# Kernel optimization log

Hardware: AMD Instinct MI355X
Metric: run time of the kernel (lower is better)

Reference implementation:

```python
import jax, jax.numpy as jnp
import numpy as np

N = 50000      # nodes
E = 600000     # edges
F_IN = 128     # input features
H = 128        # hidden
C = 40         # classes


def _glorot(key, shape):
    lim = float(np.sqrt(6.0 / (shape[0] + shape[1])))
    return jax.random.uniform(key, shape, jnp.float32, -lim, lim)


def setup_inputs() -> dict:
    key = jax.random.key(0)
    ks = jax.random.split(key, 16)
    inp = {
        "x": jax.random.normal(ks[0], (N, F_IN), jnp.float32),
        "edge_index": jax.random.randint(ks[1], (2, E), 0, N, jnp.int64),
    }
    # SAGEConv params: Wl (neighbor branch, with bias), Wr (root branch), stored [in, out]
    dims = [(F_IN, H), (H, H), (H, H)]
    for i, (din, dout) in enumerate(dims, start=1):
        inp[f"Wl{i}"] = _glorot(ks[2 * i], (din, dout))
        inp[f"bl{i}"] = jnp.zeros((dout,), jnp.float32)
        inp[f"Wr{i}"] = _glorot(ks[2 * i + 1], (din, dout))
    inp["W_lin1"] = _glorot(ks[10], (H, H))
    inp["b_lin1"] = jnp.zeros((H,), jnp.float32)
    inp["W_lin2"] = _glorot(ks[11], (H, C))
    inp["b_lin2"] = jnp.zeros((C,), jnp.float32)
    return inp


def _sage_conv(x, src, dst, Wl, bl, Wr):
    # mean-aggregate neighbor features at destination nodes
    msgs = x[src]  # [E, d] gather
    agg = jax.ops.segment_sum(msgs, dst, num_segments=N)
    deg = jax.ops.segment_sum(jnp.ones((E,), x.dtype), dst, num_segments=N)
    agg = agg / jnp.clip(deg, 1.0)[:, None]
    return agg @ Wl + bl + x @ Wr


def reference(x, edge_index, Wl1, bl1, Wr1, Wl2, bl2, Wr2, Wl3, bl3, Wr3,
              W_lin1, b_lin1, W_lin2, b_lin2):
    src, dst = edge_index[0], edge_index[1]
    h = jax.nn.relu(_sage_conv(x, src, dst, Wl1, bl1, Wr1))
    h = jax.nn.relu(_sage_conv(h, src, dst, Wl2, bl2, Wr2))
    h = jax.nn.relu(_sage_conv(h, src, dst, Wl3, bl3, Wr3))
    h = jax.nn.relu(h @ W_lin1 + b_lin1)
    # dropout: inference mode (training=False) -> identity
    logits = h @ W_lin2 + b_lin2
    return jax.nn.log_softmax(logits, axis=-1)
```

## Files before the change

### kernel.cpp

```cpp
#include <hip/hip_runtime.h>
#include <hip/hip_bf16.h>
#include <math.h>

#define NNODES 50000
#define NEDGES 600000
#define FDIM   128
#define NCLS   40
#define SLOTS  64
#define FILL_BLOCKS 1172
#define CVT_BLOCKS 6250
#define PACK_BLOCKS 62
#define ALL_TOTAL (FILL_BLOCKS + CVT_BLOCKS + PACK_BLOCKS)
#define NT64 ((NNODES + 63) / 64)

typedef __hip_bfloat16 bf16;
typedef short bf16x8 __attribute__((ext_vector_type(8)));
typedef short bf16x4 __attribute__((ext_vector_type(4)));
typedef float f32x4  __attribute__((ext_vector_type(4)));
typedef float f32x2  __attribute__((ext_vector_type(2)));
typedef unsigned u32x4 __attribute__((ext_vector_type(4)));

__device__ __forceinline__ float u2f(unsigned u) {
    union { unsigned i; float f; } cv;
    cv.i = u;
    return cv.f;
}
__device__ __forceinline__ short f2b(float f) {
    bf16 h = __float2bfloat16(f);
    return *(const short*)&h;
}
__device__ __forceinline__ float ldf(const void* p, int fp32, int idx) {
    return fp32 ? ((const float*)p)[idx]
                : __bfloat162float(((const bf16*)p)[idx]);
}
__device__ __forceinline__ int wave_is_fp32(const unsigned* p, int lane) {
    unsigned w = p[lane];
    unsigned e = (w >> 7) & 0xFFu;
    int inr = (e >= 100u && e <= 140u) ? 1 : 0;
    return (int)__popcll(__ballot(inr)) < 32;
}
__device__ __forceinline__ int lidx(int row, int col) {
    return row * 128 + ((((col >> 3) ^ (row & 15)) << 3) | (col & 7));
}

__global__ void k_all(const int* __restrict__ e32, const long long* __restrict__ e64,
                      const void* __restrict__ xin,
                      const void* Wl1, const void* Wr1, const void* Wl2,
                      const void* Wr2, const void* Wl3, const void* Wr3,
                      const void* Wlin1, const void* Wlin2,
                      const void* b1, const void* b2, const void* b3,
                      const void* b4, const void* b5,
                      int* __restrict__ cursor, int* __restrict__ edge_src,
                      bf16* __restrict__ xb,
                      bf16x8* __restrict__ packed, float* __restrict__ biasf) {
    int b = blockIdx.x, tid = threadIdx.x, lane = tid & 63;
    if (b < FILL_BLOCKS) {
        unsigned hw = ((const unsigned*)e32)[2 * lane + 1];
        int is64 = (__ballot(hw != 0u) == 0ull) ? 1 : 0;
        int i0 = b * 512 + tid;
        int i1 = i0 + 256;
        int s0 = 0, d0 = 0, s1 = 0, d1 = 0;
        bool v0 = i0 < NEDGES, v1 = i1 < NEDGES;
        if (v0) { s0 = is64 ? (int)e64[i0] : e32[i0];
                  d0 = is64 ? (int)e64[NEDGES + i0] : e32[NEDGES + i0]; }
        if (v1) { s1 = is64 ? (int)e64[i1] : e32[i1];
                  d1 = is64 ? (int)e64[NEDGES + i1] : e32[NEDGES + i1]; }
        int p0 = 0, p1 = 0;
        if (v0) p0 = atomicAdd(&cursor[d0], 1);
        if (v1) p1 = atomicAdd(&cursor[d1], 1);
        if (v0 && p0 < SLOTS) edge_src[d0 * SLOTS + p0] = s0;
        if (v1 && p1 < SLOTS) edge_src[d1 * SLOTS + p1] = s1;
        return;
    }
    if (b < FILL_BLOCKS + CVT_BLOCKS) {
        int xf = wave_is_fp32((const unsigned*)xin, lane);
        int i = (b - FILL_BLOCKS) * 256 + tid;
        if (xf) {
            float4 v = ((const float4*)xin)[i];
            bf16x4 o;
            o[0] = f2b(v.x); o[1] = f2b(v.y); o[2] = f2b(v.z); o[3] = f2b(v.w);
            ((bf16x4*)xb)[i] = o;
        } else {
            ((uint2*)xb)[i] = ((const uint2*)xin)[i];
        }
        return;
    }
    int wf = wave_is_fp32((const unsigned*)Wl1, lane);
    int lb = b - FILL_BLOCKS - CVT_BLOCKS;
    if (lb >= 59) {
        int t = (lb - 59) * 256 + tid;
        if (t >= 5 * 128) return;
        int which = t >> 7, idx = t & 127;
        const void* srcs[5] = {b1, b2, b3, b4, b5};
        int n = (which == 4) ? NCLS : 128;
        float v = 0.f;
        if (idx < n) v = ldf(srcs[which], wf, idx);
        biasf[t] = v;
        return;
    }
    int t2 = lb * 256 + tid;
    int frag = t2 >> 6;
    if (frag >= 236) return;
    int q = lane >> 4, l16 = lane & 15;
    const void* W;
    int kbase, n, ldw = 128, nvalid = 128;
    if (frag < 192) {
        int g = frag >> 6, local = frag & 63;
        int kt = local >> 3, nt = local & 7;
        const void* Wl = (g == 0) ? Wl1 : (g == 1) ? Wl2 : Wl3;
        const void* Wr = (g == 0) ? Wr1 : (g == 1) ? Wr2 : Wr3;
        W = (kt < 4) ? Wl : Wr;
        kbase = (kt & 3) * 32;
        n = nt * 16 + l16;
    } else if (frag < 224) {
        int local = frag - 192;
        int kt = local >> 3, nt = local & 7;
        W = Wlin1; kbase = kt * 32; n = nt * 16 + l16;
    } else {
        int local = frag - 224;
        int kt = local / 3, nt = local % 3;
        W = Wlin2; kbase = kt * 32; n = nt * 16 + l16;
        ldw = NCLS; nvalid = NCLS;
    }
    bf16x8 v;
#pragma unroll
    for (int j = 0; j < 8; j++) {
        float e = 0.f;
        if (n < nvalid) e = ldf(W, wf, (kbase + q * 8 + j) * ldw + n);
        v[j] = f2b(e);
    }
    packed[frag * 64 + lane] = v;
}

__device__ __forceinline__ void agg16(const bf16* __restrict__ x,
        const int* __restrict__ deg, const int* __restrict__ es,
        short* __restrict__ lds, int node0, int lane) {
    const int g = lane >> 4, c = lane & 15;
    const int gsel = lane & 48;
    int dgp[4], eip[4];
#pragma unroll
    for (int p = 0; p < 4; p++) dgp[p] = deg[node0 + p * 4 + g];
#pragma unroll
    for (int p = 0; p < 4; p++) {
        int ei = es[(node0 + p * 4 + g) * SLOTS + c];
        eip[p] = ((unsigned)ei >= NNODES) ? 0 : ei;
    }
#pragma unroll
    for (int p = 0; p < 4; p++) {
        const int dg = dgp[p];
        f32x2 acc2[4];
#pragma unroll
        for (int k = 0; k < 4; k++) acc2[k] = (f32x2){0.f, 0.f};
#pragma unroll
        for (int j = 0; j < 16; j++) {
            int idx = __shfl(eip[p], gsel | j);
            float m = (j < dg) ? 1.f : 0.f;
            f32x2 m2 = (f32x2){m, m};
            u32x4 u = *(const u32x4*)(x + (unsigned)(idx * FDIM + c * 8));
#pragma unroll
            for (int k = 0; k < 4; k++) {
                f32x2 vv = (f32x2){u2f(u[k] << 16), u2f(u[k] & 0xFFFF0000u)};
                acc2[k] += vv * m2;
            }
        }
        if (__ballot(dg > 16) != 0ull) {
            for (int jb = 16; jb < SLOTS && __ballot(dg > jb) != 0ull; jb += 16) {
                int ei2 = es[(node0 + p * 4 + g) * SLOTS + jb + c];
                if ((unsigned)ei2 >= NNODES) ei2 = 0;
                for (int j = 0; j < 16; j++) {
                    int idx = __shfl(ei2, gsel | j);
                    float m = (jb + j < dg) ? 1.f : 0.f;
                    f32x2 m2 = (f32x2){m, m};
                    u32x4 u = *(const u32x4*)(x + (unsigned)(idx * FDIM + c * 8));
#pragma unroll
                    for (int k = 0; k < 4; k++) {
                        f32x2 vv = (f32x2){u2f(u[k] << 16), u2f(u[k] & 0xFFFF0000u)};
                        acc2[k] += vv * m2;
                    }
                }
            }
        }
        float inv = (dg > 0) ? 1.f / (float)dg : 0.f;
        bf16x8 o;
#pragma unroll
        for (int k = 0; k < 4; k++) {
            o[2 * k]     = f2b(acc2[k].x * inv);
            o[2 * k + 1] = f2b(acc2[k].y * inv);
        }
        *(bf16x8*)(lds + lidx(p * 4 + g, c * 8)) = o;
    }
}

__device__ __forceinline__ void gemm16(int lane, short* __restrict__ lds,
        const bf16x8 rt[4], const bf16x8* __restrict__ packed,
        const float* __restrict__ bias) {
    const int q = lane >> 4, l16 = lane & 15;
    f32x4 acc[8];
#pragma unroll
    for (int n = 0; n < 8; n++) acc[n] = (f32x4){0.f, 0.f, 0.f, 0.f};
#pragma unroll
    for (int kt = 0; kt < 8; kt++) {
        bf16x8 a;
        if (kt < 4)
            a = *(const bf16x8*)(lds + lidx(l16, kt * 32 + q * 8));
        else
            a = rt[kt - 4];
#pragma unroll
        for (int n = 0; n < 8; n++)
            acc[n] = __builtin_amdgcn_mfma_f32_16x16x32_bf16(
                a, packed[(kt * 8 + n) * 64 + lane], acc[n], 0, 0, 0);
    }
#pragma unroll
    for (int n = 0; n < 8; n++) {
        int col = n * 16 + l16;
        float bv = bias[col];
#pragma unroll
        for (int r = 0; r < 4; r++)
            lds[lidx(q * 4 + r, col)] = f2b(fmaxf(acc[n][r] + bv, 0.f));
    }
}

__device__ __forceinline__ void store16(int rowbase, int lane,
        const short* __restrict__ lds, bf16* __restrict__ out) {
    const int g = lane >> 4, c = lane & 15;
#pragma unroll
    for (int p = 0; p < 4; p++) {
        bf16x8 v = *(const bf16x8*)(lds + lidx(p * 4 + g, c * 8));
        *(bf16x8*)(out + (unsigned)((rowbase + p * 4 + g) * FDIM + c * 8)) = v;
    }
}

__device__ __forceinline__ void head16(int rowbase, int lane,
        const short* __restrict__ h3, short* __restrict__ h1,
        const bf16x8* __restrict__ packed, const float* __restrict__ bias1,
        const float* __restrict__ bias2, float* __restrict__ out) {
    const int q = lane >> 4, l16 = lane & 15;
    f32x4 acc[8];
#pragma unroll
    for (int n = 0; n < 8; n++) acc[n] = (f32x4){0.f, 0.f, 0.f, 0.f};
#pragma unroll
    for (int kt = 0; kt < 4; kt++) {
        bf16x8 a = *(const bf16x8*)(h3 + lidx(l16, kt * 32 + q * 8));
#pragma unroll
        for (int n = 0; n < 8; n++)
            acc[n] = __builtin_amdgcn_mfma_f32_16x16x32_bf16(
                a, packed[(192 + kt * 8 + n) * 64 + lane], acc[n], 0, 0, 0);
    }
#pragma unroll
    for (int n = 0; n < 8; n++) {
        int col = n * 16 + l16;
        float bv = bias1[col];
#pragma unroll
        for (int r = 0; r < 4; r++)
            h1[lidx(q * 4 + r, col)] = f2b(fmaxf(acc[n][r] + bv, 0.f));
    }
    f32x4 acc2[3];
#pragma unroll
    for (int n = 0; n < 3; n++) acc2[n] = (f32x4){0.f, 0.f, 0.f, 0.f};
#pragma unroll
    for (int kt = 0; kt < 4; kt++) {
        bf16x8 a = *(const bf16x8*)(h1 + lidx(l16, kt * 32 + q * 8));
#pragma unroll
        for (int n = 0; n < 3; n++)
            acc2[n] = __builtin_amdgcn_mfma_f32_16x16x32_bf16(
                a, packed[(224 + kt * 3 + n) * 64 + lane], acc2[n], 0, 0, 0);
    }
    const float NEG = -1e30f;
    bool v2ok = (l16 < 8);
#pragma unroll
    for (int r = 0; r < 4; r++) {
        unsigned row = (unsigned)(rowbase + q * 4 + r);
        float v0 = acc2[0][r] + bias2[l16];
        float v1 = acc2[1][r] + bias2[16 + l16];
        float v2 = v2ok ? (acc2[2][r] + bias2[32 + l16]) : NEG;
        float m = fmaxf(fmaxf(v0, v1), v2);
#pragma unroll
        for (int mk = 1; mk < 16; mk <<= 1) m = fmaxf(m, __shfl_xor(m, mk));
        float sden = expf(v0 - m) + expf(v1 - m) + (v2ok ? expf(v2 - m) : 0.f);
#pragma unroll
        for (int mk = 1; mk < 16; mk <<= 1) sden += __shfl_xor(sden, mk);
        float l = m + logf(sden);
        out[row * NCLS + l16] = v0 - l;
        out[row * NCLS + 16 + l16] = v1 - l;
        if (v2ok) out[row * NCLS + 32 + l16] = v2 - l;
    }
}

__global__ void __launch_bounds__(256)
k_layer(const bf16* __restrict__ src, const int* __restrict__ deg,
        const int* __restrict__ edge_src, const bf16x8* __restrict__ packed,
        const float* __restrict__ bias, bf16* __restrict__ out) {
    __shared__ __align__(16) short lds[4 * 16 * 128];
    const int lane = threadIdx.x & 63, wave = threadIdx.x >> 6;
    const int rowbase = blockIdx.x * 64 + wave * 16;
    if (rowbase >= NNODES) return;
    short* wlds = lds + wave * 16 * 128;
    const int q = lane >> 4, l16 = lane & 15;
    bf16x8 rt[4];
#pragma unroll
    for (int kt = 0; kt < 4; kt++)
        rt[kt] = *(const bf16x8*)(src +
                     (unsigned)((rowbase + l16) * FDIM + kt * 32 + q * 8));
    agg16(src, deg, edge_src, wlds, rowbase, lane);
    gemm16(lane, wlds, rt, packed, bias);
    store16(rowbase, lane, wlds, out);
}

__global__ void __launch_bounds__(256)
k_layer3head(const bf16* __restrict__ src, const int* __restrict__ deg,
             const int* __restrict__ edge_src, const bf16x8* __restrict__ packed,
             const float* __restrict__ biasf, float* __restrict__ out) {
    __shared__ __align__(16) short h3[4 * 16 * 128];
    __shared__ __align__(16) short h1[4 * 16 * 128];
    const int lane = threadIdx.x & 63, wave = threadIdx.x >> 6;
    const int rowbase = blockIdx.x * 64 + wave * 16;
    if (rowbase >= NNODES) return;
    short* wh3 = h3 + wave * 16 * 128;
    short* wh1 = h1 + wave * 16 * 128;
    const int q = lane >> 4, l16 = lane & 15;
    bf16x8 rt[4];
#pragma unroll
    for (int kt = 0; kt < 4; kt++)
        rt[kt] = *(const bf16x8*)(src +
                     (unsigned)((rowbase + l16) * FDIM + kt * 32 + q * 8));
    agg16(src, deg, edge_src, wh3, rowbase, lane);
    gemm16(lane, wh3, rt, packed + 128 * 64, biasf + 256);
    head16(rowbase, lane, wh3, wh1, packed, biasf + 384, biasf + 512, out);
}

extern "C" void kernel_launch(void* const* d_in, const int* in_sizes, int n_in,
                              void* d_out, int out_size, void* d_ws, size_t ws_size,
                              hipStream_t stream) {
    char* ws = (char*)d_ws;
    size_t off = 0;
    auto take = [&](size_t bytes) {
        void* pp = ws + off;
        off = (off + bytes + 255) & ~(size_t)255;
        return pp;
    };
    const int* e32 = (const int*)d_in[1];
    const long long* e64 = (const long long*)d_in[1];
    int* cursor    = (int*)take(NNODES * 4);
    int* edge_src  = (int*)take((size_t)NNODES * SLOTS * 4);
    bf16x8* packed = (bf16x8*)take(236 * 64 * 16);
    float* biasf   = (float*)take(5 * 128 * 4);
    bf16* xb       = (bf16*)take((size_t)NNODES * FDIM * 2);
    bf16* bufA     = (bf16*)take((size_t)NNODES * FDIM * 2);
    float* outp    = (float*)d_out;
    bf16* bufB     = xb;

    hipMemsetAsync(cursor, 0, NNODES * 4, stream);
    k_all<<<ALL_TOTAL, 256, 0, stream>>>(
        e32, e64, d_in[0], d_in[2], d_in[4], d_in[5], d_in[7], d_in[8],
        d_in[10], d_in[11], d_in[13], d_in[3], d_in[6], d_in[9], d_in[12],
        d_in[14], cursor, edge_src, xb, packed, biasf);

    k_layer<<<NT64, 256, 0, stream>>>(xb, cursor, edge_src, packed, biasf, bufA);
    k_layer<<<NT64, 256, 0, stream>>>(bufA, cursor, edge_src,
                                      packed + 64 * 64, biasf + 128, bufB);
    k_layer3head<<<NT64, 256, 0, stream>>>(bufB, cursor, edge_src,
                                           packed, biasf, outp);
}
```

Before: 253.4 us.

## Split each 16-row tile across two cooperating waves for aggregation and GEMM

Each block now handles 16 nodes with two waves. Each wave aggregates 8 nodes' neighbours, and each wave computes half of the output columns of the fused GEMM, synchronising through shared LDS. The aim is more parallelism per tile and shorter per-wave latency chains, giving more blocks and better latency hiding in the gather-bound layers. In exchange it adds block-level barriers, and the small logits head runs on only one wave.

```diff
diff --git a/kernel.cpp b/kernel.cpp
--- a/kernel.cpp
+++ b/kernel.cpp
@@ -11,7 +11,7 @@
 #define CVT_BLOCKS 6250
 #define PACK_BLOCKS 62
 #define ALL_TOTAL (FILL_BLOCKS + CVT_BLOCKS + PACK_BLOCKS)
-#define NT64 ((NNODES + 63) / 64)
+#define NT16 (NNODES / 16)
 
 typedef __hip_bfloat16 bf16;
 typedef short bf16x8 __attribute__((ext_vector_type(8)));
@@ -132,21 +132,22 @@
     packed[frag * 64 + lane] = v;
 }
 
-__device__ __forceinline__ void agg16(const bf16* __restrict__ x,
+__device__ __forceinline__ void agg8(const bf16* __restrict__ x,
         const int* __restrict__ deg, const int* __restrict__ es,
-        short* __restrict__ lds, int node0, int lane) {
+        short* __restrict__ lds, int node00, int wave, int lane) {
     const int g = lane >> 4, c = lane & 15;
     const int gsel = lane & 48;
-    int dgp[4], eip[4];
-#pragma unroll
-    for (int p = 0; p < 4; p++) dgp[p] = deg[node0 + p * 4 + g];
-#pragma unroll
-    for (int p = 0; p < 4; p++) {
-        int ei = es[(node0 + p * 4 + g) * SLOTS + c];
+    const int nbase = node00 + wave * 8;
+    int dgp[2], eip[2];
+#pragma unroll
+    for (int p = 0; p < 2; p++) dgp[p] = deg[nbase + p * 4 + g];
+#pragma unroll
+    for (int p = 0; p < 2; p++) {
+        int ei = es[(nbase + p * 4 + g) * SLOTS + c];
         eip[p] = ((unsigned)ei >= NNODES) ? 0 : ei;
     }
 #pragma unroll
-    for (int p = 0; p < 4; p++) {
+    for (int p = 0; p < 2; p++) {
         const int dg = dgp[p];
         f32x2 acc2[4];
 #pragma unroll
@@ -165,7 +166,7 @@
         }
         if (__ballot(dg > 16) != 0ull) {
             for (int jb = 16; jb < SLOTS && __ballot(dg > jb) != 0ull; jb += 16) {
-                int ei2 = es[(node0 + p * 4 + g) * SLOTS + jb + c];
+                int ei2 = es[(nbase + p * 4 + g) * SLOTS + jb + c];
                 if ((unsigned)ei2 >= NNODES) ei2 = 0;
                 for (int j = 0; j < 16; j++) {
                     int idx = __shfl(ei2, gsel | j);
@@ -187,17 +188,17 @@
             o[2 * k]     = f2b(acc2[k].x * inv);
             o[2 * k + 1] = f2b(acc2[k].y * inv);
         }
-        *(bf16x8*)(lds + lidx(p * 4 + g, c * 8)) = o;
-    }
-}
-
-__device__ __forceinline__ void gemm16(int lane, short* __restrict__ lds,
-        const bf16x8 rt[4], const bf16x8* __restrict__ packed,
-        const float* __restrict__ bias) {
+        *(bf16x8*)(lds + lidx(wave * 8 + p * 4 + g, c * 8)) = o;
+    }
+}
+
+__device__ __forceinline__ void gemm_half(int lane, int wave,
+        short* __restrict__ lds, const bf16x8 rt[4],
+        const bf16x8* __restrict__ packed, const float* __restrict__ bias) {
     const int q = lane >> 4, l16 = lane & 15;
-    f32x4 acc[8];
-#pragma unroll
-    for (int n = 0; n < 8; n++) acc[n] = (f32x4){0.f, 0.f, 0.f, 0.f};
+    f32x4 acc[4];
+#pragma unroll
+    for (int n = 0; n < 4; n++) acc[n] = (f32x4){0.f, 0.f, 0.f, 0.f};
 #pragma unroll
     for (int kt = 0; kt < 8; kt++) {
         bf16x8 a;
@@ -206,54 +207,59 @@
         else
             a = rt[kt - 4];
 #pragma unroll
-        for (int n = 0; n < 8; n++)
+        for (int n = 0; n < 4; n++)
             acc[n] = __builtin_amdgcn_mfma_f32_16x16x32_bf16(
-                a, packed[(kt * 8 + n) * 64 + lane], acc[n], 0, 0, 0);
-    }
-#pragma unroll
-    for (int n = 0; n < 8; n++) {
-        int col = n * 16 + l16;
+                a, packed[(kt * 8 + wave * 4 + n) * 64 + lane], acc[n], 0, 0, 0);
+    }
+    __syncthreads();
+#pragma unroll
+    for (int n = 0; n < 4; n++) {
+        int col = (wave * 4 + n) * 16 + l16;
         float bv = bias[col];
 #pragma unroll
         for (int r = 0; r < 4; r++)
             lds[lidx(q * 4 + r, col)] = f2b(fmaxf(acc[n][r] + bv, 0.f));
     }
-}
-
-__device__ __forceinline__ void store16(int rowbase, int lane,
+    __syncthreads();
+}
+
+__device__ __forceinline__ void store_half(int rowbase, int lane, int wave,
         const short* __restrict__ lds, bf16* __restrict__ out) {
     const int g = lane >> 4, c = lane & 15;
 #pragma unroll
-    for (int p = 0; p < 4; p++) {
+    for (int pp = 0; pp < 2; pp++) {
+        int p = wave * 2 + pp;
         bf16x8 v = *(const bf16x8*)(lds + lidx(p * 4 + g, c * 8));
         *(bf16x8*)(out + (unsigned)((rowbase + p * 4 + g) * FDIM + c * 8)) = v;
     }
 }
 
-__device__ __forceinline__ void head16(int rowbase, int lane,
+__device__ __forceinline__ void head(int rowbase, int lane, int wave,
         const short* __restrict__ h3, short* __restrict__ h1,
         const bf16x8* __restrict__ packed, const float* __restrict__ bias1,
         const float* __restrict__ bias2, float* __restrict__ out) {
     const int q = lane >> 4, l16 = lane & 15;
-    f32x4 acc[8];
-#pragma unroll
-    for (int n = 0; n < 8; n++) acc[n] = (f32x4){0.f, 0.f, 0.f, 0.f};
+    f32x4 acc[4];
+#pragma unroll
+    for (int n = 0; n < 4; n++) acc[n] = (f32x4){0.f, 0.f, 0.f, 0.f};
 #pragma unroll
     for (int kt = 0; kt < 4; kt++) {
         bf16x8 a = *(const bf16x8*)(h3 + lidx(l16, kt * 32 + q * 8));
 #pragma unroll
-        for (int n = 0; n < 8; n++)
+        for (int n = 0; n < 4; n++)
             acc[n] = __builtin_amdgcn_mfma_f32_16x16x32_bf16(
-                a, packed[(192 + kt * 8 + n) * 64 + lane], acc[n], 0, 0, 0);
-    }
-#pragma unroll
-    for (int n = 0; n < 8; n++) {
-        int col = n * 16 + l16;
+                a, packed[(192 + kt * 8 + wave * 4 + n) * 64 + lane], acc[n], 0, 0, 0);
+    }
+#pragma unroll
+    for (int n = 0; n < 4; n++) {
+        int col = (wave * 4 + n) * 16 + l16;
         float bv = bias1[col];
 #pragma unroll
         for (int r = 0; r < 4; r++)
             h1[lidx(q * 4 + r, col)] = f2b(fmaxf(acc[n][r] + bv, 0.f));
     }
+    __syncthreads();
+    if (wave != 0) return;
     f32x4 acc2[3];
 #pragma unroll
     for (int n = 0; n < 3; n++) acc2[n] = (f32x4){0.f, 0.f, 0.f, 0.f};
@@ -286,46 +292,43 @@
     }
 }
 
-__global__ void __launch_bounds__(256)
+__global__ void __launch_bounds__(128)
 k_layer(const bf16* __restrict__ src, const int* __restrict__ deg,
         const int* __restrict__ edge_src, const bf16x8* __restrict__ packed,
         const float* __restrict__ bias, bf16* __restrict__ out) {
-    __shared__ __align__(16) short lds[4 * 16 * 128];
+    __shared__ __align__(16) short lds[16 * 128];
     const int lane = threadIdx.x & 63, wave = threadIdx.x >> 6;
-    const int rowbase = blockIdx.x * 64 + wave * 16;
-    if (rowbase >= NNODES) return;
-    short* wlds = lds + wave * 16 * 128;
+    const int rowbase = blockIdx.x * 16;
     const int q = lane >> 4, l16 = lane & 15;
     bf16x8 rt[4];
 #pragma unroll
     for (int kt = 0; kt < 4; kt++)
         rt[kt] = *(const bf16x8*)(src +
                      (unsigned)((rowbase + l16) * FDIM + kt * 32 + q * 8));
-    agg16(src, deg, edge_src, wlds, rowbase, lane);
-    gemm16(lane, wlds, rt, packed, bias);
-    store16(rowbase, lane, wlds, out);
-}
-
-__global__ void __launch_bounds__(256)
+    agg8(src, deg, edge_src, lds, rowbase, wave, lane);
+    __syncthreads();
+    gemm_half(lane, wave, lds, rt, packed, bias);
+    store_half(rowbase, lane, wave, lds, out);
+}
+
+__global__ void __launch_bounds__(128)
 k_layer3head(const bf16* __restrict__ src, const int* __restrict__ deg,
              const int* __restrict__ edge_src, const bf16x8* __restrict__ packed,
              const float* __restrict__ biasf, float* __restrict__ out) {
-    __shared__ __align__(16) short h3[4 * 16 * 128];
-    __shared__ __align__(16) short h1[4 * 16 * 128];
+    __shared__ __align__(16) short h3[16 * 128];
+    __shared__ __align__(16) short h1[16 * 128];
     const int lane = threadIdx.x & 63, wave = threadIdx.x >> 6;
-    const int rowbase = blockIdx.x * 64 + wave * 16;
-    if (rowbase >= NNODES) return;
-    short* wh3 = h3 + wave * 16 * 128;
-    short* wh1 = h1 + wave * 16 * 128;
+    const int rowbase = blockIdx.x * 16;
     const int q = lane >> 4, l16 = lane & 15;
     bf16x8 rt[4];
 #pragma unroll
     for (int kt = 0; kt < 4; kt++)
         rt[kt] = *(const bf16x8*)(src +
                      (unsigned)((rowbase + l16) * FDIM + kt * 32 + q * 8));
-    agg16(src, deg, edge_src, wh3, rowbase, lane);
-    gemm16(lane, wh3, rt, packed + 128 * 64, biasf + 256);
-    head16(rowbase, lane, wh3, wh1, packed, biasf + 384, biasf + 512, out);
+    agg8(src, deg, edge_src, h3, rowbase, wave, lane);
+    __syncthreads();
+    gemm_half(lane, wave, h3, rt, packed + 128 * 64, biasf + 256);
+    head(rowbase, lane, wave, h3, h1, packed, biasf + 384, biasf + 512, out);
 }
 
 extern "C" void kernel_launch(void* const* d_in, const int* in_sizes, int n_in,
@@ -355,9 +358,9 @@
         d_in[10], d_in[11], d_in[13], d_in[3], d_in[6], d_in[9], d_in[12],
         d_in[14], cursor, edge_src, xb, packed, biasf);
 
-    k_layer<<<NT64, 256, 0, stream>>>(xb, cursor, edge_src, packed, biasf, bufA);
-    k_layer<<<NT64, 256, 0, stream>>>(bufA, cursor, edge_src,
+    k_layer<<<NT16, 128, 0, stream>>>(xb, cursor, edge_src, packed, biasf, bufA);
+    k_layer<<<NT16, 128, 0, stream>>>(bufA, cursor, edge_src,
                                       packed + 64 * 64, biasf + 128, bufB);
-    k_layer3head<<<NT64, 256, 0, stream>>>(bufB, cursor, edge_src,
+    k_layer3head<<<NT16, 128, 0, stream>>>(bufB, cursor, edge_src,
                                            packed, biasf, outp);
 }
```

New measurement: 230.0 us. 9.2% less time.
